# Kernel tuning notes

Measured on AMD Instinct MI355X. Metric: run time of the kernel, lower is better.

The kernel has to match this reference:

```python
import jax, jax.numpy as jnp
import numpy as np

BETA = 0.25
NUM_EMBEDDINGS = 8192
EMBEDDING_DIM = 256


def setup_inputs() -> dict:
    key = jax.random.key(0)
    k1, k2 = jax.random.split(key)
    z = jax.random.normal(k1, (16, EMBEDDING_DIM, 32, 32), dtype=jnp.float32)
    lim = 1.0 / NUM_EMBEDDINGS
    emb = jax.random.uniform(k2, (NUM_EMBEDDINGS, EMBEDDING_DIM),
                             minval=-lim, maxval=lim, dtype=jnp.float32)
    return {"z": z, "emb": emb}


def reference(z, emb):
    # z: [B, C, H, W] with C == embedding_dim; emb: [K, C]
    B, C, H, W = z.shape
    zp = jnp.transpose(z, (0, 2, 3, 1))          # [B, H, W, C]
    zf = zp.reshape(-1, C)                        # [N, C]
    # squared-L2 distances via expansion: ||z||^2 + ||e||^2 - 2 z.e
    d = (jnp.sum(zf * zf, axis=1, keepdims=True)
         + jnp.sum(emb * emb, axis=1)
         - 2.0 * zf @ emb.T)                      # [N, K]
    idx = jnp.argmin(d, axis=1)                   # [N]
    z_q = emb[idx].reshape(zp.shape)              # [B, H, W, C]
    # losses (commitment uses detached z; embedding loss uses detached z_q)
    commitment_loss = BETA * jnp.mean((jax.lax.stop_gradient(zp) - z_q) ** 2)
    embedding_loss = jnp.mean((zp - jax.lax.stop_gradient(z_q)) ** 2)
    vq_loss = commitment_loss + embedding_loss
    # straight-through estimator
    z_q_st = zp + jax.lax.stop_gradient(z_q - zp)
    return (jnp.transpose(z_q_st, (0, 3, 1, 2)), vq_loss, idx)
```

## Files before the change

kernel.cpp:

```cpp
#include <hip/hip_runtime.h>

#define BATCH   16
#define CDIM    256
#define NPTS    16384
#define KCODES  8192
#define NELEM   4194304
#define ESCALE  4096.0f
#define MARGIN  0.5f
#define PPB     32
#define NCHUNK  8

typedef _Float16 f16;
typedef _Float16 f16x8 __attribute__((ext_vector_type(8)));
typedef _Float16 f16x4 __attribute__((ext_vector_type(4)));
typedef float    f32x4 __attribute__((ext_vector_type(4)));

__device__ __forceinline__ void gload16(const void* g, void* l) {
    __builtin_amdgcn_global_load_lds(
        (const __attribute__((address_space(1))) unsigned int*)g,
        (__attribute__((address_space(3))) unsigned int*)l, 16, 0, 0);
}

__global__ __launch_bounds__(256) void k_prep_z(const float* __restrict__ z,
                                                f16* __restrict__ z16,
                                                float* __restrict__ zz,
                                                float* __restrict__ zc) {
    __shared__ f16 tile[64][264];
    __shared__ float tile32[64][260];
    __shared__ float red[4][64];
    const int n0 = blockIdx.x * 64;
    const int b = n0 >> 10, hw0 = n0 & 1023;
    const int p = threadIdx.x & 63, g = threadIdx.x >> 6;
    const float* zb = z + b * 262144 + hw0 + p;
    float s = 0.f;
    for (int c = g * 64; c < g * 64 + 64; ++c) {
        float v = zb[c * 1024];
        s = fmaf(v, v, s);
        tile[p][c] = (f16)v;
        tile32[p][c] = v;
    }
    red[g][p] = s;
    __syncthreads();
    if (g == 0) zz[n0 + p] = (red[0][p] + red[1][p]) + (red[2][p] + red[3][p]);
    const int r = threadIdx.x >> 2, q = threadIdx.x & 3;
    f16* dst = z16 + (size_t)(n0 + r) * 256 + q * 64;
    #pragma unroll
    for (int j = 0; j < 8; ++j)
        *(f16x8*)(dst + j * 8) = *(const f16x8*)(&tile[r][q * 64 + j * 8]);
    if (zc) {
        const int w = threadIdx.x >> 6, l = threadIdx.x & 63;
        #pragma unroll
        for (int rr = 0; rr < 16; ++rr) {
            const int row = w * 16 + rr;
            *(float4*)(zc + (size_t)(n0 + row) * 256 + l * 4) =
                *(const float4*)(&tile32[row][l * 4]);
        }
    }
}

__global__ __launch_bounds__(256) void k_prep_e(const float* __restrict__ emb,
                                                f16* __restrict__ e16) {
    const int i = (blockIdx.x * 256 + threadIdx.x) * 4;
    float4 v = *(const float4*)(emb + i);
    f16x4 o = {(f16)(v.x * ESCALE), (f16)(v.y * ESCALE),
               (f16)(v.z * ESCALE), (f16)(v.w * ESCALE)};
    *(f16x4*)(e16 + i) = o;
}

__device__ __forceinline__ void stage_tile(const f16* zg, const f16* eg,
                                           f16* Ab, f16* Bb, int t, int kt) {
    #pragma unroll
    for (int pp = 0; pp < 4; ++pp) {
        const int gi  = pp * 512 + t;
        const int row = gi >> 3;
        const int kc  = (gi & 7) ^ (row & 7);
        const size_t goff = (size_t)row * 256 + (size_t)kt * 64 + kc * 8;
        gload16(zg + goff, (char*)Ab + gi * 16);
        gload16(eg + goff, (char*)Bb + gi * 16);
    }
}

__global__ __launch_bounds__(512, 2) void k_gemm(const f16* __restrict__ z16,
                                                 const f16* __restrict__ e16,
                                                 f16* __restrict__ gmaxT) {
    __shared__ f16 As[2][16384];
    __shared__ f16 Bs[2][16384];
    const int bid = blockIdx.x;
    const int bm = bid >> 5, bn = bid & 31;
    const size_t m0 = (size_t)bm * 256, n0 = (size_t)bn * 256;
    const int t = threadIdx.x, lane = t & 63, w = t >> 6;
    const int wm = w >> 2, wn = w & 3;

    const f16* zg = z16 + m0 * 256;
    const f16* eg = e16 + n0 * 256;

    f32x4 acc[8][4] = {};

    stage_tile(zg, eg, As[0], Bs[0], t, 0);
    __syncthreads();

    for (int kt = 0; kt < 4; ++kt) {
        const int buf = kt & 1;
        if (kt < 3) stage_tile(zg, eg, As[buf ^ 1], Bs[buf ^ 1], t, kt + 1);
        const char* Ab = (const char*)As[buf];
        const char* Bb = (const char*)Bs[buf];
        #pragma unroll
        for (int kk = 0; kk < 2; ++kk) {
            f16x8 a[8], bf[4];
            const int kc = kk * 4 + (lane >> 4);
            #pragma unroll
            for (int mr = 0; mr < 8; ++mr) {
                const int row = wm * 128 + mr * 16 + (lane & 15);
                a[mr] = *(const f16x8*)(Ab + row * 128 + ((kc ^ (row & 7)) << 4));
            }
            #pragma unroll
            for (int nr = 0; nr < 4; ++nr) {
                const int row = wn * 64 + nr * 16 + (lane & 15);
                bf[nr] = *(const f16x8*)(Bb + row * 128 + ((kc ^ (row & 7)) << 4));
            }
            #pragma unroll
            for (int mr = 0; mr < 8; ++mr)
                #pragma unroll
                for (int nr = 0; nr < 4; ++nr)
                    acc[mr][nr] = __builtin_amdgcn_mfma_f32_16x16x32_f16(
                        a[mr], bf[nr], acc[mr][nr], 0, 0, 0);
        }
        __syncthreads();
    }

    const int g = bn * 4 + wn;
    #pragma unroll
    for (int mr = 0; mr < 8; ++mr) {
        #pragma unroll
        for (int q = 0; q < 4; ++q) {
            float v = acc[mr][0][q];
            v = fmaxf(v, acc[mr][1][q]);
            v = fmaxf(v, acc[mr][2][q]);
            v = fmaxf(v, acc[mr][3][q]);
            v = fmaxf(v, __shfl_xor(v, 1));
            v = fmaxf(v, __shfl_xor(v, 2));
            v = fmaxf(v, __shfl_xor(v, 4));
            v = fmaxf(v, __shfl_xor(v, 8));
            if ((lane & 15) == 0) {
                const int p = wm * 128 + mr * 16 + ((lane >> 4) << 2) + q;
                gmaxT[(size_t)g * 16384 + m0 + p] = (f16)v;
            }
        }
    }
}

__global__ __launch_bounds__(256) void k_pmax(const f16* __restrict__ gmaxT,
                                              float* __restrict__ thr) {
    const int n = blockIdx.x * 256 + threadIdx.x;
    float m = -1e30f;
    #pragma unroll 16
    for (int g = 0; g < 128; ++g)
        m = fmaxf(m, (float)gmaxT[(size_t)g * 16384 + n]);
    thr[n] = m - MARGIN;
}

__global__ __launch_bounds__(256) void k_build(const f16* __restrict__ gmaxT,
                                               const float* __restrict__ thr,
                                               unsigned* __restrict__ cnt,
                                               unsigned* __restrict__ list) {
    __shared__ unsigned wsum[4];
    const int g = blockIdx.x;
    const int t = threadIdx.x, lane = t & 63, w = t >> 6;
    const f16* row = gmaxT + (size_t)g * 16384;
    unsigned* gl = list + (size_t)g * 16384;
    unsigned run = 0;
    for (int c = 0; c < 64; ++c) {
        const int n = c * 256 + t;
        const bool f = (float)row[n] >= thr[n];
        const unsigned long long mk = __ballot(f);
        if (lane == 0) wsum[w] = (unsigned)__popcll(mk);
        __syncthreads();
        const unsigned w0 = wsum[0], w1 = wsum[1], w2 = wsum[2], w3 = wsum[3];
        if (f) {
            const unsigned wexcl = (w > 0 ? w0 : 0u) + (w > 1 ? w1 : 0u) + (w > 2 ? w2 : 0u);
            const unsigned rank = (unsigned)__popcll(mk & ((1ull << lane) - 1ull));
            gl[run + wexcl + rank] = (unsigned)n;
        }
        run += w0 + w1 + w2 + w3;
        __syncthreads();
    }
    if (t == 0) cnt[g] = run;
}

__global__ __launch_bounds__(256) void k_rescore2(const float* __restrict__ emb,
                                                  const float* __restrict__ zc,
                                                  const float* __restrict__ zz,
                                                  const unsigned* __restrict__ cnt,
                                                  const unsigned* __restrict__ list,
                                                  unsigned long long* __restrict__ best) {
    __shared__ float es[64 * 260];
    __shared__ float zs[4][256];
    const int g = blockIdx.x >> 3, c = blockIdx.x & 7;
    const unsigned nct = cnt[g];
    if (nct <= (unsigned)(c * PPB)) return;

    const int t = threadIdx.x, lane = t & 63, w = t >> 6;
    {
        const float* eg = emb + (size_t)g * 64 * 256;
        for (int i = t * 4; i < 16384; i += 1024) {
            const float4 v = *(const float4*)(eg + i);
            const int row = i >> 8, col = i & 255;
            *(float4*)(&es[row * 260 + col]) = v;
        }
    }
    __syncthreads();

    const unsigned* gl = list + g * 16384;
    for (unsigned base = c * PPB; base < nct; base += NCHUNK * PPB) {
        #pragma unroll 1
        for (int j = 0; j < 8; ++j) {
            const unsigned i = base + w * 8 + j;
            if (i >= nct || i >= base + PPB) continue;
            const unsigned n = gl[i];
            const float4 zv = *(const float4*)(zc + (size_t)n * 256 + lane * 4);
            *(float4*)(&zs[w][lane * 4]) = zv;
            const float zzv = zz[n];
            const float4* zr = (const float4*)(&zs[w][0]);
            const float4* er = (const float4*)(&es[lane * 260]);
            float4 a = {0.f, 0.f, 0.f, 0.f};
            #pragma unroll 8
            for (int c4 = 0; c4 < 64; ++c4) {
                const float4 e4 = er[c4];
                const float4 z4 = zr[c4];
                a.x = fmaf(z4.x, e4.x, a.x);
                a.y = fmaf(z4.y, e4.y, a.y);
                a.z = fmaf(z4.z, e4.z, a.z);
                a.w = fmaf(z4.w, e4.w, a.w);
            }
            const float dot = (a.x + a.y) + (a.z + a.w);
            const float d = fmaf(-2.f, dot, zzv);
            unsigned long long key =
                ((unsigned long long)__float_as_uint(d) << 32) | (unsigned)(g * 64 + lane);
            #pragma unroll
            for (int s = 1; s < 64; s <<= 1) {
                const unsigned long long o = __shfl_xor(key, s);
                if (o < key) key = o;
            }
            if (lane == 0) atomicMin(&best[n], key);
        }
    }
}

__global__ __launch_bounds__(256) void k_rescore(const float* __restrict__ z,
                                                 const float* __restrict__ emb,
                                                 const float* __restrict__ zz,
                                                 const f16* __restrict__ gmaxT,
                                                 unsigned long long* __restrict__ best) {
    __shared__ float zsh[16][260];
    const int n0 = blockIdx.x * 16;
    const int b = n0 >> 10, hw0 = n0 & 1023;
    const int t = threadIdx.x, lane = t & 63, w = t >> 6;
    {
        const int p = t & 15, cq = t >> 4;
        const float* zp = z + (size_t)b * 262144 + hw0 + p;
        #pragma unroll
        for (int c = cq * 16; c < cq * 16 + 16; ++c)
            zsh[p][c] = zp[(size_t)c * 1024];
    }
    __syncthreads();
    for (int p = w; p < 16; p += 4) {
        const int n = n0 + p;
        const float g0 = (float)gmaxT[(size_t)lane * 16384 + n];
        const float g1 = (float)gmaxT[(size_t)(lane + 64) * 16384 + n];
        float m = fmaxf(g0, g1);
        #pragma unroll
        for (int s = 1; s < 64; s <<= 1) m = fmaxf(m, __shfl_xor(m, s));
        const float thr = m - MARGIN;
        unsigned long long f0 = __ballot(g0 >= thr);
        unsigned long long f1 = __ballot(g1 >= thr);
        const float zzv = zz[n];
        const float4* zr = (const float4*)(&zsh[p][0]);
        unsigned long long key = ~0ull;
        while (f0 | f1) {
            int g;
            if (f0) { g = __ffsll(f0) - 1; f0 &= f0 - 1; }
            else    { g = 64 + __ffsll(f1) - 1; f1 &= f1 - 1; }
            const float4* er = (const float4*)(emb + ((size_t)(g * 64 + lane) << 8));
            float4 a = {0.f, 0.f, 0.f, 0.f};
            #pragma unroll 8
            for (int c4 = 0; c4 < 64; ++c4) {
                const float4 e4 = er[c4];
                const float4 z4 = zr[c4];
                a.x = fmaf(z4.x, e4.x, a.x);
                a.y = fmaf(z4.y, e4.y, a.y);
                a.z = fmaf(z4.z, e4.z, a.z);
                a.w = fmaf(z4.w, e4.w, a.w);
            }
            const float dot = (a.x + a.y) + (a.z + a.w);
            const float d = fmaf(-2.f, dot, zzv);
            const unsigned long long kk =
                ((unsigned long long)__float_as_uint(d) << 32) | (unsigned)(g * 64 + lane);
            if (kk < key) key = kk;
        }
        #pragma unroll
        for (int s = 1; s < 64; s <<= 1) {
            const unsigned long long o = __shfl_xor(key, s);
            if (o < key) key = o;
        }
        if (lane == 0) best[n] = key;
    }
}

__global__ __launch_bounds__(256) void k_out(const float* __restrict__ z,
                                             const float* __restrict__ emb,
                                             const unsigned long long* __restrict__ best,
                                             float* __restrict__ out0,
                                             float* __restrict__ out2,
                                             double* __restrict__ loss) {
    const int n0 = blockIdx.x * 64;
    const int b = n0 >> 10, hw0 = n0 & 1023;
    const int p = threadIdx.x & 63, cg = threadIdx.x >> 6;
    const int n = n0 + p;
    const int idx = (int)(unsigned)(best[n] & 0xffffffffull);
    if (threadIdx.x < 64)
        out2[n0 + threadIdx.x] =
            (float)(int)(unsigned)(best[n0 + threadIdx.x] & 0xffffffffull);

    const float* zb = z + b * 262144 + hw0 + p;
    float*       ob = out0 + b * 262144 + hw0 + p;
    const float* eb = emb + idx * 256;
    double ls = 0.0;
    #pragma unroll 4
    for (int c = cg * 64; c < cg * 64 + 64; ++c) {
        float zp = zb[c * 1024];
        float e  = eb[c];
        float diff = e - zp;
        ob[c * 1024] = zp + diff;
        float l = zp - e;
        ls += (double)l * (double)l;
    }
    __shared__ double red[256];
    red[threadIdx.x] = ls;
    __syncthreads();
    for (int s = 128; s > 0; s >>= 1) {
        if (threadIdx.x < s) red[threadIdx.x] += red[threadIdx.x + s];
        __syncthreads();
    }
    if (threadIdx.x == 0) atomicAdd(loss, red[0]);
}

__global__ void k_loss(const double* __restrict__ loss, float* __restrict__ out1) {
    float m = (float)(*loss / (double)NELEM);
    out1[0] = 0.25f * m + m;
}

extern "C" void kernel_launch(void* const* d_in, const int* in_sizes, int n_in,
                              void* d_out, int out_size, void* d_ws, size_t ws_size,
                              hipStream_t stream) {
    const float* z   = (const float*)d_in[0];
    const float* emb = (const float*)d_in[1];
    float* out  = (float*)d_out;
    float* out0 = out;
    float* out1 = out + NELEM;
    float* out2 = out + NELEM + 1;

    f16* z16    = (f16*)out0;
    f16* e16    = (f16*)((char*)out0 + 8388608);
    f16* gmaxT  = (f16*)((char*)out0 + 12582912);
    unsigned* list = (unsigned*)out0;
    float* thr  = (float*)((char*)out0 + 8388608);

    const size_t ZC_BYTES = 16777216;
    const bool fast = ws_size >= ZC_BYTES + 65536 + 131072 + 1024;

    if (fast) {
        float* zc = (float*)d_ws;
        float* zzp = (float*)((char*)d_ws + ZC_BYTES);
        unsigned long long* best =
            (unsigned long long*)((char*)d_ws + ZC_BYTES + 65536);
        unsigned* cnt = (unsigned*)((char*)d_ws + ZC_BYTES + 65536 + 131072);
        double* loss  = (double*)((char*)d_ws + ZC_BYTES + 65536 + 131072 + 512);

        hipMemsetAsync(best, 0xFF, NPTS * 8, stream);
        hipMemsetAsync(loss, 0, 8, stream);
        k_prep_z<<<256, 256, 0, stream>>>(z, z16, zzp, zc);
        k_prep_e<<<2048, 256, 0, stream>>>(emb, e16);
        k_gemm<<<2048, 512, 0, stream>>>(z16, e16, gmaxT);
        k_pmax<<<64, 256, 0, stream>>>(gmaxT, thr);
        k_build<<<128, 256, 0, stream>>>(gmaxT, thr, cnt, list);
        k_rescore2<<<128 * NCHUNK, 256, 0, stream>>>(emb, zc, zzp, cnt, list, best);
        k_out<<<256, 256, 0, stream>>>(z, emb, best, out0, out2, loss);
        k_loss<<<1, 1, 0, stream>>>(loss, out1);
    } else {
        float* zzp = (float*)d_ws;
        unsigned long long* best =
            (unsigned long long*)((char*)d_ws + 65536);
        double* loss = (double*)((char*)d_ws + 65536 + 131072);

        hipMemsetAsync(loss, 0, 8, stream);
        k_prep_z<<<256, 256, 0, stream>>>(z, z16, zzp, nullptr);
        k_prep_e<<<2048, 256, 0, stream>>>(emb, e16);
        k_gemm<<<2048, 512, 0, stream>>>(z16, e16, gmaxT);
        k_rescore<<<1024, 256, 0, stream>>>(z, emb, zzp, gmaxT, best);
        k_out<<<256, 256, 0, stream>>>(z, emb, best, out0, out2, loss);
        k_loss<<<1, 1, 0, stream>>>(loss, out1);
    }
}
```

Measured before the change: 242.4 us.

## Restructure GEMM main loop into ping-pong phases with explicit waits and priority

Rewrites the k_gemm K-loop so both LDS buffers are prefetched up front, and each k-step splits the A fragment loads into two halves interleaved with MFMA bursts. Explicit s_barrier, waitcnt, sched_barrier and setprio calls replace the compiler-placed __syncthreads. The goal is to overlap LDS reads and global-to-LDS staging with MFMA work and to keep waves in lockstep, in the style of an HipKittens 8-wave ping-pong schedule. It adds more barriers per iteration and depends on hand-placed waitcnts being correct. Tile prefetch now waits on all outstanding vmcnt before reusing a buffer.

```diff
diff --git a/kernel.cpp b/kernel.cpp
--- a/kernel.cpp
+++ b/kernel.cpp
@@ -97,35 +97,72 @@
     f32x4 acc[8][4] = {};
 
     stage_tile(zg, eg, As[0], Bs[0], t, 0);
-    __syncthreads();
-
+    __builtin_amdgcn_sched_barrier(0);
+    asm volatile("s_waitcnt vmcnt(0)" ::: "memory");
+    __builtin_amdgcn_sched_barrier(0);
+    stage_tile(zg, eg, As[1], Bs[1], t, 1);
+    __builtin_amdgcn_sched_barrier(0);
+    __builtin_amdgcn_s_barrier();
+
+    #pragma unroll
     for (int kt = 0; kt < 4; ++kt) {
-        const int buf = kt & 1;
-        if (kt < 3) stage_tile(zg, eg, As[buf ^ 1], Bs[buf ^ 1], t, kt + 1);
-        const char* Ab = (const char*)As[buf];
-        const char* Bb = (const char*)Bs[buf];
+        const char* Ab = (const char*)As[kt & 1];
+        const char* Bb = (const char*)Bs[kt & 1];
         #pragma unroll
         for (int kk = 0; kk < 2; ++kk) {
-            f16x8 a[8], bf[4];
             const int kc = kk * 4 + (lane >> 4);
-            #pragma unroll
-            for (int mr = 0; mr < 8; ++mr) {
-                const int row = wm * 128 + mr * 16 + (lane & 15);
-                a[mr] = *(const f16x8*)(Ab + row * 128 + ((kc ^ (row & 7)) << 4));
-            }
+            f16x8 bfr[4], alo[4], ahi[4];
             #pragma unroll
             for (int nr = 0; nr < 4; ++nr) {
                 const int row = wn * 64 + nr * 16 + (lane & 15);
-                bf[nr] = *(const f16x8*)(Bb + row * 128 + ((kc ^ (row & 7)) << 4));
-            }
-            #pragma unroll
-            for (int mr = 0; mr < 8; ++mr)
+                bfr[nr] = *(const f16x8*)(Bb + row * 128 + ((kc ^ (row & 7)) << 4));
+            }
+            #pragma unroll
+            for (int mr = 0; mr < 4; ++mr) {
+                const int row = wm * 128 + mr * 16 + (lane & 15);
+                alo[mr] = *(const f16x8*)(Ab + row * 128 + ((kc ^ (row & 7)) << 4));
+            }
+            __builtin_amdgcn_s_barrier();
+            asm volatile("s_waitcnt lgkmcnt(0)" ::: "memory");
+            __builtin_amdgcn_sched_barrier(0);
+            __builtin_amdgcn_s_setprio(1);
+            #pragma unroll
+            for (int mr = 0; mr < 4; ++mr)
                 #pragma unroll
                 for (int nr = 0; nr < 4; ++nr)
                     acc[mr][nr] = __builtin_amdgcn_mfma_f32_16x16x32_f16(
-                        a[mr], bf[nr], acc[mr][nr], 0, 0, 0);
-        }
-        __syncthreads();
+                        alo[mr], bfr[nr], acc[mr][nr], 0, 0, 0);
+            __builtin_amdgcn_s_setprio(0);
+            __builtin_amdgcn_sched_barrier(0);
+            __builtin_amdgcn_s_barrier();
+            #pragma unroll
+            for (int mr = 0; mr < 4; ++mr) {
+                const int row = wm * 128 + (mr + 4) * 16 + (lane & 15);
+                ahi[mr] = *(const f16x8*)(Ab + row * 128 + ((kc ^ (row & 7)) << 4));
+            }
+            __builtin_amdgcn_s_barrier();
+            asm volatile("s_waitcnt lgkmcnt(0)" ::: "memory");
+            __builtin_amdgcn_sched_barrier(0);
+            __builtin_amdgcn_s_setprio(1);
+            #pragma unroll
+            for (int mr = 0; mr < 4; ++mr)
+                #pragma unroll
+                for (int nr = 0; nr < 4; ++nr)
+                    acc[mr + 4][nr] = __builtin_amdgcn_mfma_f32_16x16x32_f16(
+                        ahi[mr], bfr[nr], acc[mr + 4][nr], 0, 0, 0);
+            __builtin_amdgcn_s_setprio(0);
+            __builtin_amdgcn_sched_barrier(0);
+            __builtin_amdgcn_s_barrier();
+        }
+        if (kt < 3) {
+            asm volatile("s_waitcnt vmcnt(0)" ::: "memory");
+            __builtin_amdgcn_sched_barrier(0);
+        }
+        if (kt < 2) {
+            stage_tile(zg, eg, (f16*)As[kt & 1], (f16*)Bs[kt & 1], t, kt + 2);
+            __builtin_amdgcn_sched_barrier(0);
+        }
+        __builtin_amdgcn_s_barrier();
     }
 
     const int g = bn * 4 + wn;
```

Result: no change. 246.7 us (+1.8%).
